# Kernel optimization log

Measured on AMD Instinct MI355X. Metric: run time of the kernel, lower is better.

Reference implementation:

```python
import jax, jax.numpy as jnp
import numpy as np

N, F_IN, HID, HEADS, NC, E, NG = 50000, 128, 64, 4, 8, 800000, 512


def setup_inputs() -> dict:
    key = jax.random.key(0)
    ks = jax.random.split(key, 16)
    x = jax.random.normal(ks[0], (N, F_IN), dtype=jnp.float32)
    # edges with src != dst so every node's incoming set is exactly {neighbors, self-loop}
    dst = jax.random.randint(ks[1], (E,), 0, N, dtype=jnp.int64)
    off = jax.random.randint(ks[2], (E,), 1, N, dtype=jnp.int64)
    src = (dst + off) % N
    edge_index = jnp.stack([src, dst])
    batch = jnp.sort(jax.random.randint(ks[3], (N,), 0, NG, dtype=jnp.int64))
    g = 1.0 / np.sqrt(F_IN)
    W1 = jax.random.uniform(ks[4], (F_IN, HEADS * HID), jnp.float32, -g, g)
    att_src1 = jax.random.normal(ks[5], (HEADS, HID), jnp.float32) * 0.1
    att_dst1 = jax.random.normal(ks[6], (HEADS, HID), jnp.float32) * 0.1
    b1 = jnp.zeros((HEADS * HID,), jnp.float32)
    g2 = 1.0 / np.sqrt(HEADS * HID)
    W2 = jax.random.uniform(ks[7], (HEADS * HID, HID), jnp.float32, -g2, g2)
    att_src2 = jax.random.normal(ks[8], (1, HID), jnp.float32) * 0.1
    att_dst2 = jax.random.normal(ks[9], (1, HID), jnp.float32) * 0.1
    b2 = jnp.zeros((HID,), jnp.float32)
    g3 = 1.0 / np.sqrt(HID)
    lin_w = jax.random.uniform(ks[10], (HID, NC), jnp.float32, -g3, g3)
    lin_b = jnp.zeros((NC,), jnp.float32)
    return dict(x=x, edge_index=edge_index, batch=batch, W1=W1, att_src1=att_src1,
                att_dst1=att_dst1, b1=b1, W2=W2, att_src2=att_src2, att_dst2=att_dst2,
                b2=b2, lin_w=lin_w, lin_b=lin_b)


def gat_layer(x, src, dst, W, att_s, att_d, bias, heads, out_ch):
    # PyG GATConv: h = x @ W, e_ij = LeakyReLU(a_s.h_j + a_d.h_i), softmax over dst groups
    h = (x @ W).reshape(-1, heads, out_ch)                    # [N,H,C]
    a_s = jnp.einsum('nhc,hc->nh', h, att_s)                  # [N,H]
    a_d = jnp.einsum('nhc,hc->nh', h, att_d)
    e = jax.nn.leaky_relu(a_s[src] + a_d[dst], 0.2)           # [Ef,H]
    m = jax.ops.segment_max(e, dst, num_segments=N)           # stable segment softmax
    ex = jnp.exp(e - m[dst])
    s = jax.ops.segment_sum(ex, dst, num_segments=N)
    alpha = ex / (s[dst] + 1e-16)                             # [Ef,H]
    msg = h[src] * alpha[:, :, None]                          # [Ef,H,C]
    out = jax.ops.segment_sum(msg, dst, num_segments=N)       # [N,H,C]
    return out.reshape(-1, heads * out_ch) + bias, alpha


def reference(x, edge_index, batch, W1, att_src1, att_dst1, b1,
              W2, att_src2, att_dst2, b2, lin_w, lin_b):
    loops = jnp.arange(N, dtype=edge_index.dtype)
    src = jnp.concatenate([edge_index[0], loops])             # add self-loops (PyG default)
    dst = jnp.concatenate([edge_index[1], loops])
    h, alpha1 = gat_layer(x, src, dst, W1, att_src1, att_dst1, b1, HEADS, HID)
    h = jax.nn.relu(h)
    # conv2 on edge_index_1 (already has self-loops; PyG remove+add is a no-op here)
    h, alpha2 = gat_layer(h, src, dst, W2, att_src2, att_dst2, b2, 1, HID)
    h = jax.nn.relu(h)
    sums = jax.ops.segment_sum(h, batch, num_segments=NG)     # global_mean_pool
    cnt = jax.ops.segment_sum(jnp.ones((N,), h.dtype), batch, num_segments=NG)
    pooled = sums / jnp.maximum(cnt, 1.0)[:, None]
    # dropout is identity in eval mode
    return pooled @ lin_w + lin_b
```

## Files before the change

### kernel.cpp

```cpp
#include <hip/hip_runtime.h>

#define F_IN 128
#define HID 64
#define HEADS 4
#define NC 8

typedef __bf16 bf16_t;
typedef bf16_t bf16x8 __attribute__((ext_vector_type(8)));
typedef float f32x4 __attribute__((ext_vector_type(4)));

union BF8 { bf16x8 v; ushort u[8]; };


__device__ __forceinline__ ushort f2bf(float f) {
    uint u = __float_as_uint(f);
    return (ushort)((u + 0x7fffu + ((u >> 16) & 1u)) >> 16);
}
__device__ __forceinline__ float bf2f(ushort h) {
    return __uint_as_float(((uint)h) << 16);
}
__device__ __forceinline__ float edgew(float e) {
    e = (e > 0.f) ? e : 0.2f * e;
    return __expf(e);
}


__global__ void k_init(int* __restrict__ deg, int N, int* __restrict__ counts, int NG) {
    int i = blockIdx.x * blockDim.x + threadIdx.x;
    if (i < N) deg[i] = 1;
    if (i < NG) counts[i] = 0;
}

__global__ void k_count(const int* __restrict__ ei, int E, int* __restrict__ deg,
                        const int* __restrict__ batch, int N, int* __restrict__ counts) {
    int i = blockIdx.x * blockDim.x + threadIdx.x;
    if (i < E) atomicAdd(&deg[ei[E + i]], 1);
    if (i < N) atomicAdd(&counts[batch[i]], 1);
}

__global__ __launch_bounds__(1024) void k_scan_part(const int* __restrict__ v,
                                                    int* __restrict__ excl,
                                                    int* __restrict__ bsum, int n) {
    __shared__ int buf[1024];
    int tid = threadIdx.x;
    int i = blockIdx.x * 1024 + tid;
    int val = (i < n) ? v[i] : 0;
    buf[tid] = val;
    __syncthreads();
    for (int off = 1; off < 1024; off <<= 1) {
        int t = (tid >= off) ? buf[tid - off] : 0;
        __syncthreads();
        buf[tid] += t;
        __syncthreads();
    }
    if (i < n) excl[i] = buf[tid] - val;
    if (tid == 1023) bsum[blockIdx.x] = buf[1023];
}

__global__ __launch_bounds__(1024) void k_scan_bsum(const int* __restrict__ bsum,
                                                    int* __restrict__ boff, int nb,
                                                    int* __restrict__ total_out) {
    __shared__ int buf[1024];
    int tid = threadIdx.x;
    int val = (tid < nb) ? bsum[tid] : 0;
    buf[tid] = val;
    __syncthreads();
    for (int off = 1; off < 1024; off <<= 1) {
        int t = (tid >= off) ? buf[tid - off] : 0;
        __syncthreads();
        buf[tid] += t;
        __syncthreads();
    }
    if (tid < nb) boff[tid] = buf[tid] - val;
    if (tid == 1023) total_out[0] = buf[1023];
}

__global__ void k_scan_add_self(int* __restrict__ rowstart, const int* __restrict__ boff,
                                int* __restrict__ cursor, int* __restrict__ csr, int n) {
    int i = blockIdx.x * blockDim.x + threadIdx.x;
    if (i < n) {
        int rs = rowstart[i] + boff[i >> 10];
        rowstart[i] = rs;
        csr[rs] = i;
        cursor[i] = 1;
    }
}

__global__ __launch_bounds__(1024) void k_scan(const int* __restrict__ v, int* __restrict__ excl, int n) {
    __shared__ int buf[1024];
    int tid = threadIdx.x;
    int val = (tid < n) ? v[tid] : 0;
    buf[tid] = val;
    __syncthreads();
    for (int off = 1; off < 1024; off <<= 1) {
        int t = (tid >= off) ? buf[tid - off] : 0;
        __syncthreads();
        buf[tid] += t;
        __syncthreads();
    }
    if (tid < n) excl[tid] = buf[tid] - val;
    if (tid == 1023) excl[n] = buf[1023];
}

__global__ void k_scatter(const int* __restrict__ ei, int E, const int* __restrict__ rowstart,
                          int* __restrict__ cursor, int* __restrict__ csr) {
    int e = blockIdx.x * blockDim.x + threadIdx.x;
    if (e < E) {
        int d = ei[E + e], s = ei[e];
        int pos = atomicAdd(&cursor[d], 1);
        csr[rowstart[d] + pos] = s;
    }
}

__global__ void k_pack(const float* __restrict__ W1, const float* __restrict__ W2,
                       ushort* __restrict__ w1hi, ushort* __restrict__ w1lo,
                       ushort* __restrict__ w2hi, ushort* __restrict__ w2lo) {
    int i = blockIdx.x * blockDim.x + threadIdx.x;
    if (i < 128 * 256) {
        int k = i >> 8, n = i & 255;
        int cy = n >> 7, ct = (n >> 4) & 7, c = n & 15, kc = k >> 5, ls = (k >> 3) & 3, j = k & 7;
        size_t off = ((((size_t)cy * 8 + ct) * 4 + kc) * 64 + (ls * 16 + c)) * 8 + j;
        float w = W1[i];
        ushort hi = f2bf(w);
        w1hi[off] = hi; w1lo[off] = f2bf(w - bf2f(hi));
    }
    if (i < 256 * 64) {
        int k = i >> 6, n = i & 63;
        int ct = n >> 4, c = n & 15, kc = k >> 5, ls = (k >> 3) & 3, j = k & 7;
        size_t off = (((size_t)ct * 8 + kc) * 64 + (ls * 16 + c)) * 8 + j;
        float w = W2[i];
        ushort hi = f2bf(w);
        w2hi[off] = hi; w2lo[off] = f2bf(w - bf2f(hi));
    }
}

__global__ __launch_bounds__(256) void k_gemm1(const float* __restrict__ x,
                                               const ushort* __restrict__ w1hi,
                                               const ushort* __restrict__ w1lo,
                                               const float* __restrict__ atts,
                                               const float* __restrict__ attd,
                                               ushort* __restrict__ h1b,
                                               float* __restrict__ as1, float* __restrict__ ad1,
                                               int N) {
    __shared__ __align__(16) ushort lhi[16384];
    __shared__ __align__(16) ushort llo[16384];
    int tid = threadIdx.x;
    int cy = blockIdx.y;
    {
        float4* dh = (float4*)lhi; const float4* sh = (const float4*)(w1hi + (size_t)cy * 16384);
        float4* dl = (float4*)llo; const float4* sl = (const float4*)(w1lo + (size_t)cy * 16384);
        #pragma unroll
        for (int i = 0; i < 8; i++) {
            dh[tid + i * 256] = sh[tid + i * 256];
            dl[tid + i * 256] = sl[tid + i * 256];
        }
    }
    __syncthreads();
    int w = tid >> 6, l = tid & 63;
    int lc = l & 15, lk = l >> 4;
    int rbase = blockIdx.x * 256 + w * 64;

    f32x4 acc[4][8];
    #pragma unroll
    for (int mt = 0; mt < 4; mt++)
        #pragma unroll
        for (int ct = 0; ct < 8; ct++) acc[mt][ct] = (f32x4){0.f, 0.f, 0.f, 0.f};

    #pragma unroll
    for (int kc = 0; kc < 4; kc++) {
        BF8 ahi[4], alo[4];
        #pragma unroll
        for (int mt = 0; mt < 4; mt++) {
            int row = rbase + mt * 16 + lc;
            float4 v0 = {0.f, 0.f, 0.f, 0.f}, v1 = v0;
            if (row < N) {
                const float* xp = x + (size_t)row * F_IN + kc * 32 + lk * 8;
                v0 = *(const float4*)xp; v1 = *(const float4*)(xp + 4);
            }
            float vals[8] = {v0.x, v0.y, v0.z, v0.w, v1.x, v1.y, v1.z, v1.w};
            #pragma unroll
            for (int j = 0; j < 8; j++) {
                ushort h = f2bf(vals[j]);
                ahi[mt].u[j] = h;
                alo[mt].u[j] = f2bf(vals[j] - bf2f(h));
            }
        }
        #pragma unroll
        for (int ct = 0; ct < 8; ct++) {
            int boff = ((ct * 4 + kc) * 64 + l) * 8;
            bf16x8 bhi = *(const bf16x8*)(lhi + boff);
            bf16x8 blo = *(const bf16x8*)(llo + boff);
            #pragma unroll
            for (int mt = 0; mt < 4; mt++) {
                acc[mt][ct] = __builtin_amdgcn_mfma_f32_16x16x32_bf16(ahi[mt].v, bhi, acc[mt][ct], 0, 0, 0);
                acc[mt][ct] = __builtin_amdgcn_mfma_f32_16x16x32_bf16(alo[mt].v, bhi, acc[mt][ct], 0, 0, 0);
                acc[mt][ct] = __builtin_amdgcn_mfma_f32_16x16x32_bf16(ahi[mt].v, blo, acc[mt][ct], 0, 0, 0);
            }
        }
    }
    #pragma unroll
    for (int mt = 0; mt < 4; mt++) {
        int rowb = rbase + mt * 16 + lk * 4;
        #pragma unroll
        for (int ct = 0; ct < 8; ct++) {
            int col = cy * 128 + ct * 16 + lc;
            #pragma unroll
            for (int r = 0; r < 4; r++) {
                int row = rowb + r;
                if (row < N) h1b[(size_t)row * 256 + col] = f2bf(acc[mt][ct][r]);
            }
        }
        #pragma unroll
        for (int hh = 0; hh < 2; hh++) {
            float s[4] = {0.f, 0.f, 0.f, 0.f}, d[4] = {0.f, 0.f, 0.f, 0.f};
            #pragma unroll
            for (int cq = 0; cq < 4; cq++) {
                int ct = hh * 4 + cq;
                int col = cy * 128 + ct * 16 + lc;
                float av = atts[col], dv = attd[col];
                #pragma unroll
                for (int r = 0; r < 4; r++) { s[r] += acc[mt][ct][r] * av; d[r] += acc[mt][ct][r] * dv; }
            }
            #pragma unroll
            for (int r = 0; r < 4; r++) {
                #pragma unroll
                for (int off = 1; off < 16; off <<= 1) {
                    s[r] += __shfl_xor(s[r], off);
                    d[r] += __shfl_xor(d[r], off);
                }
            }
            if (lc == 0) {
                int head = cy * 2 + hh;
                #pragma unroll
                for (int r = 0; r < 4; r++) {
                    int row = rowb + r;
                    if (row < N) { as1[row * 4 + head] = s[r]; ad1[row * 4 + head] = d[r]; }
                }
            }
        }
    }
}

__global__ __launch_bounds__(256) void k_gemm2(const float* __restrict__ xin,
                                               const ushort* __restrict__ w2hi,
                                               const ushort* __restrict__ w2lo,
                                               const float* __restrict__ atts,
                                               const float* __restrict__ attd,
                                               ushort* __restrict__ h2b,
                                               float* __restrict__ as2, float* __restrict__ ad2,
                                               int N) {
    __shared__ __align__(16) ushort lhi[16384];
    __shared__ __align__(16) ushort llo[16384];
    int tid = threadIdx.x;
    {
        float4* dh = (float4*)lhi; const float4* sh = (const float4*)w2hi;
        float4* dl = (float4*)llo; const float4* sl = (const float4*)w2lo;
        #pragma unroll
        for (int i = 0; i < 8; i++) {
            dh[tid + i * 256] = sh[tid + i * 256];
            dl[tid + i * 256] = sl[tid + i * 256];
        }
    }
    __syncthreads();
    int w = tid >> 6, l = tid & 63;
    int lc = l & 15, lk = l >> 4;
    int rbase = blockIdx.x * 256 + w * 64;

    f32x4 acc[4][4];
    #pragma unroll
    for (int mt = 0; mt < 4; mt++)
        #pragma unroll
        for (int ct = 0; ct < 4; ct++) acc[mt][ct] = (f32x4){0.f, 0.f, 0.f, 0.f};

    #pragma unroll
    for (int kc = 0; kc < 8; kc++) {
        BF8 ahi[4], alo[4];
        #pragma unroll
        for (int mt = 0; mt < 4; mt++) {
            int row = rbase + mt * 16 + lc;
            float4 v0 = {0.f, 0.f, 0.f, 0.f}, v1 = v0;
            if (row < N) {
                const float* xp = xin + (size_t)row * 256 + kc * 32 + lk * 8;
                v0 = *(const float4*)xp; v1 = *(const float4*)(xp + 4);
            }
            float vals[8] = {v0.x, v0.y, v0.z, v0.w, v1.x, v1.y, v1.z, v1.w};
            #pragma unroll
            for (int j = 0; j < 8; j++) {
                ushort h = f2bf(vals[j]);
                ahi[mt].u[j] = h;
                alo[mt].u[j] = f2bf(vals[j] - bf2f(h));
            }
        }
        #pragma unroll
        for (int ct = 0; ct < 4; ct++) {
            int boff = ((ct * 8 + kc) * 64 + l) * 8;
            bf16x8 bhi = *(const bf16x8*)(lhi + boff);
            bf16x8 blo = *(const bf16x8*)(llo + boff);
            #pragma unroll
            for (int mt = 0; mt < 4; mt++) {
                acc[mt][ct] = __builtin_amdgcn_mfma_f32_16x16x32_bf16(ahi[mt].v, bhi, acc[mt][ct], 0, 0, 0);
                acc[mt][ct] = __builtin_amdgcn_mfma_f32_16x16x32_bf16(alo[mt].v, bhi, acc[mt][ct], 0, 0, 0);
                acc[mt][ct] = __builtin_amdgcn_mfma_f32_16x16x32_bf16(ahi[mt].v, blo, acc[mt][ct], 0, 0, 0);
            }
        }
    }
    #pragma unroll
    for (int mt = 0; mt < 4; mt++) {
        int rowb = rbase + mt * 16 + lk * 4;
        #pragma unroll
        for (int ct = 0; ct < 4; ct++) {
            int col = ct * 16 + lc;
            #pragma unroll
            for (int r = 0; r < 4; r++) {
                int row = rowb + r;
                if (row < N) h2b[(size_t)row * 64 + col] = f2bf(acc[mt][ct][r]);
            }
        }
        float s[4] = {0.f, 0.f, 0.f, 0.f}, d[4] = {0.f, 0.f, 0.f, 0.f};
        #pragma unroll
        for (int ct = 0; ct < 4; ct++) {
            int col = ct * 16 + lc;
            float av = atts[col], dv = attd[col];
            #pragma unroll
            for (int r = 0; r < 4; r++) { s[r] += acc[mt][ct][r] * av; d[r] += acc[mt][ct][r] * dv; }
        }
        #pragma unroll
        for (int r = 0; r < 4; r++) {
            #pragma unroll
            for (int off = 1; off < 16; off <<= 1) {
                s[r] += __shfl_xor(s[r], off);
                d[r] += __shfl_xor(d[r], off);
            }
        }
        if (lc == 0) {
            #pragma unroll
            for (int r = 0; r < 4; r++) {
                int row = rowb + r;
                if (row < N) { as2[row] = s[r]; ad2[row] = d[r]; }
            }
        }
    }
}


__global__ __launch_bounds__(256) void k_agg1(const ushort* __restrict__ h1b,
                                              const float* __restrict__ as, const float* __restrict__ ad,
                                              const int* __restrict__ rowstart, const int* __restrict__ csr,
                                              const float* __restrict__ b1,
                                              float* __restrict__ out1, int N) {
    int n = blockIdx.x * 4 + (threadIdx.x >> 6);
    int lane = threadIdx.x & 63;
    if (n >= N) return;
    int head = lane >> 4;
    int coff = lane * 4;
    float adv = ad[n * 4 + head];
    int beg = rowstart[n], end = rowstart[n + 1];
    float a0 = 0.f, a1 = 0.f, a2 = 0.f, a3 = 0.f, ssum = 0.f;
    int j = beg;
    for (; j + 4 <= end; j += 4) {
        int s0 = csr[j + 0], s1 = csr[j + 1], s2 = csr[j + 2], s3 = csr[j + 3];
        float e0 = as[s0 * 4 + head], e1 = as[s1 * 4 + head];
        float e2 = as[s2 * 4 + head], e3 = as[s3 * 4 + head];
        ushort4 v0 = *(const ushort4*)(h1b + (size_t)s0 * 256 + coff);
        ushort4 v1 = *(const ushort4*)(h1b + (size_t)s1 * 256 + coff);
        ushort4 v2 = *(const ushort4*)(h1b + (size_t)s2 * 256 + coff);
        ushort4 v3 = *(const ushort4*)(h1b + (size_t)s3 * 256 + coff);
        float w0 = edgew(e0 + adv), w1 = edgew(e1 + adv);
        float w2 = edgew(e2 + adv), w3 = edgew(e3 + adv);
        ssum += (w0 + w1) + (w2 + w3);
        a0 += w0 * bf2f(v0.x) + w1 * bf2f(v1.x) + w2 * bf2f(v2.x) + w3 * bf2f(v3.x);
        a1 += w0 * bf2f(v0.y) + w1 * bf2f(v1.y) + w2 * bf2f(v2.y) + w3 * bf2f(v3.y);
        a2 += w0 * bf2f(v0.z) + w1 * bf2f(v1.z) + w2 * bf2f(v2.z) + w3 * bf2f(v3.z);
        a3 += w0 * bf2f(v0.w) + w1 * bf2f(v1.w) + w2 * bf2f(v2.w) + w3 * bf2f(v3.w);
    }
    for (; j < end; j++) {
        int s0 = csr[j];
        float w0 = edgew(as[s0 * 4 + head] + adv);
        ushort4 v0 = *(const ushort4*)(h1b + (size_t)s0 * 256 + coff);
        ssum += w0;
        a0 += w0 * bf2f(v0.x); a1 += w0 * bf2f(v0.y);
        a2 += w0 * bf2f(v0.z); a3 += w0 * bf2f(v0.w);
    }
    float inv = 1.f / ssum;
    float o0 = a0 * inv + b1[coff + 0];
    float o1 = a1 * inv + b1[coff + 1];
    float o2 = a2 * inv + b1[coff + 2];
    float o3 = a3 * inv + b1[coff + 3];
    float4 o;
    o.x = o0 > 0.f ? o0 : 0.f; o.y = o1 > 0.f ? o1 : 0.f;
    o.z = o2 > 0.f ? o2 : 0.f; o.w = o3 > 0.f ? o3 : 0.f;
    *(float4*)(out1 + (size_t)n * 256 + coff) = o;
}

__global__ __launch_bounds__(256) void k_agg2(const ushort* __restrict__ h2b,
                                              const float* __restrict__ as, const float* __restrict__ ad,
                                              const int* __restrict__ rowstart, const int* __restrict__ csr,
                                              const float* __restrict__ b2,
                                              float* __restrict__ out2, int N) {
    int n = blockIdx.x * 4 + (threadIdx.x >> 6);
    int lane = threadIdx.x & 63;
    if (n >= N) return;
    float adv = ad[n];
    int beg = rowstart[n], end = rowstart[n + 1];
    float acc = 0.f, ssum = 0.f;
    int j = beg;
    for (; j + 4 <= end; j += 4) {
        int s0 = csr[j + 0], s1 = csr[j + 1], s2 = csr[j + 2], s3 = csr[j + 3];
        float e0 = as[s0], e1 = as[s1], e2 = as[s2], e3 = as[s3];
        ushort v0 = h2b[(size_t)s0 * 64 + lane];
        ushort v1 = h2b[(size_t)s1 * 64 + lane];
        ushort v2 = h2b[(size_t)s2 * 64 + lane];
        ushort v3 = h2b[(size_t)s3 * 64 + lane];
        float w0 = edgew(e0 + adv), w1 = edgew(e1 + adv);
        float w2 = edgew(e2 + adv), w3 = edgew(e3 + adv);
        ssum += (w0 + w1) + (w2 + w3);
        acc += w0 * bf2f(v0) + w1 * bf2f(v1) + w2 * bf2f(v2) + w3 * bf2f(v3);
    }
    for (; j < end; j++) {
        int s0 = csr[j];
        float w0 = edgew(as[s0] + adv);
        ssum += w0;
        acc += w0 * bf2f(h2b[(size_t)s0 * 64 + lane]);
    }
    float o = acc / ssum + b2[lane];
    out2[(size_t)n * 64 + lane] = o > 0.f ? o : 0.f;
}


__global__ __launch_bounds__(64) void k_pool(const float* __restrict__ out2,
                                             const int* __restrict__ gstart,
                                             const float* __restrict__ lin_w,
                                             const float* __restrict__ lin_b,
                                             float* __restrict__ out, int NG) {
    __shared__ float mean[64];
    int g = blockIdx.x;
    int lane = threadIdx.x;
    int beg = gstart[g], end = gstart[g + 1];
    float s = 0.f;
    for (int n = beg; n < end; n++) s += out2[(size_t)n * 64 + lane];
    float cnt = (float)(end - beg);
    mean[lane] = s / fmaxf(cnt, 1.f);
    __syncthreads();
    if (lane < NC) {
        float acc = lin_b[lane];
        #pragma unroll
        for (int c = 0; c < 64; c++) acc += mean[c] * lin_w[c * NC + lane];
        out[g * NC + lane] = acc;
    }
}


extern "C" void kernel_launch(void* const* d_in, const int* in_sizes, int n_in,
                              void* d_out, int out_size, void* d_ws, size_t ws_size,
                              hipStream_t stream) {
    const float* x      = (const float*)d_in[0];
    const int*   ei     = (const int*)d_in[1];
    const int*   batch  = (const int*)d_in[2];
    const float* W1     = (const float*)d_in[3];
    const float* att_s1 = (const float*)d_in[4];
    const float* att_d1 = (const float*)d_in[5];
    const float* b1     = (const float*)d_in[6];
    const float* W2     = (const float*)d_in[7];
    const float* att_s2 = (const float*)d_in[8];
    const float* att_d2 = (const float*)d_in[9];
    const float* b2     = (const float*)d_in[10];
    const float* lin_w  = (const float*)d_in[11];
    const float* lin_b  = (const float*)d_in[12];
    float* out = (float*)d_out;

    const int N  = in_sizes[0] / F_IN;
    const int E  = in_sizes[1] / 2;
    const int NG = out_size / NC;
    const int NE = E + N;
    const int NB = (N + 1023) / 1024;

    char* p = (char*)d_ws;
    auto alloc = [&](size_t bytes) { char* r = p; p += (bytes + 255) & ~(size_t)255; return r; };
    ushort* h1b     = (ushort*)alloc(sizeof(ushort) * (size_t)N * 256);
    float*  out1    = (float*)alloc(sizeof(float) * (size_t)N * 256);
    ushort* h2b     = (ushort*)alloc(sizeof(ushort) * (size_t)N * 64);
    float*  out2    = (float*)alloc(sizeof(float) * (size_t)N * 64);
    float*  as1     = (float*)alloc(sizeof(float) * (size_t)N * 4);
    float*  ad1     = (float*)alloc(sizeof(float) * (size_t)N * 4);
    float*  as2     = (float*)alloc(sizeof(float) * (size_t)N);
    float*  ad2     = (float*)alloc(sizeof(float) * (size_t)N);
    int*    rowstart= (int*)alloc(sizeof(int) * (size_t)(N + 1));
    int*    itmp    = (int*)alloc(sizeof(int) * (size_t)N);
    int*    csr     = (int*)alloc(sizeof(int) * (size_t)NE);
    int*    counts  = (int*)alloc(sizeof(int) * (size_t)NG);
    int*    gstart  = (int*)alloc(sizeof(int) * (size_t)(NG + 1));
    int*    bsum    = (int*)alloc(sizeof(int) * 1024);
    int*    boff    = (int*)alloc(sizeof(int) * 1024);
    ushort* w1hi    = (ushort*)alloc(sizeof(ushort) * 32768);
    ushort* w1lo    = (ushort*)alloc(sizeof(ushort) * 32768);
    ushort* w2hi    = (ushort*)alloc(sizeof(ushort) * 16384);
    ushort* w2lo    = (ushort*)alloc(sizeof(ushort) * 16384);

    int bs = 256;
    k_pack<<<128, 256, 0, stream>>>(W1, W2, w1hi, w1lo, w2hi, w2lo);
    k_init<<<(N + bs - 1) / bs, bs, 0, stream>>>(itmp, N, counts, NG);
    k_count<<<(E + bs - 1) / bs, bs, 0, stream>>>(ei, E, itmp, batch, N, counts);
    k_scan_part<<<NB, 1024, 0, stream>>>(itmp, rowstart, bsum, N);
    k_scan_bsum<<<1, 1024, 0, stream>>>(bsum, boff, NB, rowstart + N);
    k_scan_add_self<<<(N + 1023) / 1024, 1024, 0, stream>>>(rowstart, boff, itmp, csr, N);
    k_scan<<<1, 1024, 0, stream>>>(counts, gstart, NG);
    k_scatter<<<(E + bs - 1) / bs, bs, 0, stream>>>(ei, E, rowstart, itmp, csr);

    k_gemm1<<<dim3((N + 255) / 256, 2), 256, 0, stream>>>(x, w1hi, w1lo, att_s1, att_d1, h1b, as1, ad1, N);
    k_agg1<<<(N + 3) / 4, 256, 0, stream>>>(h1b, as1, ad1, rowstart, csr, b1, out1, N);

    k_gemm2<<<(N + 255) / 256, 256, 0, stream>>>(out1, w2hi, w2lo, att_s2, att_d2, h2b, as2, ad2, N);
    k_agg2<<<(N + 3) / 4, 256, 0, stream>>>(h2b, as2, ad2, rowstart, csr, b2, out2, N);

    k_pool<<<NG, 64, 0, stream>>>(out2, gstart, lin_w, lin_b, out, NG);
}
```

Measured before the change: 323.8 us.

## Store layer-1 output as bf16, fuse setup kernels, deepen gather unroll

Layer-1 aggregation now writes its ReLU output as bf16 instead of fp32. This halves that intermediate's write and read traffic and lets gemm2 load bf16 directly, dropping the on-the-fly hi/lo split and one of three MFMAs per tile. The weight pack and init kernels are merged, and the two small scans run as two blocks of one launch, which removes two launches. The aggregation gather loops are unrolled to 8 edges to keep more loads in flight. The cost is lower precision on the layer-2 input, since it is no longer split-bf16 compensated.

```diff
diff --git a/kernel.cpp b/kernel.cpp
--- a/kernel.cpp
+++ b/kernel.cpp
@@ -24,11 +24,29 @@
     return __expf(e);
 }
 
-
-__global__ void k_init(int* __restrict__ deg, int N, int* __restrict__ counts, int NG) {
+__global__ void k_setup(const float* __restrict__ W1, const float* __restrict__ W2,
+                        ushort* __restrict__ w1hi, ushort* __restrict__ w1lo,
+                        ushort* __restrict__ w2hi, ushort* __restrict__ w2lo,
+                        int* __restrict__ deg, int N, int* __restrict__ counts, int NG) {
     int i = blockIdx.x * blockDim.x + threadIdx.x;
     if (i < N) deg[i] = 1;
     if (i < NG) counts[i] = 0;
+    if (i < 128 * 256) {
+        int k = i >> 8, n = i & 255;
+        int cy = n >> 7, ct = (n >> 4) & 7, c = n & 15, kc = k >> 5, ls = (k >> 3) & 3, j = k & 7;
+        size_t off = ((((size_t)cy * 8 + ct) * 4 + kc) * 64 + (ls * 16 + c)) * 8 + j;
+        float w = W1[i];
+        ushort hi = f2bf(w);
+        w1hi[off] = hi; w1lo[off] = f2bf(w - bf2f(hi));
+    }
+    if (i < 256 * 64) {
+        int k = i >> 6, n = i & 63;
+        int ct = n >> 4, c = n & 15, kc = k >> 5, ls = (k >> 3) & 3, j = k & 7;
+        size_t off = (((size_t)ct * 8 + kc) * 64 + (ls * 16 + c)) * 8 + j;
+        float w = W2[i];
+        ushort hi = f2bf(w);
+        w2hi[off] = hi; w2lo[off] = f2bf(w - bf2f(hi));
+    }
 }
 
 __global__ void k_count(const int* __restrict__ ei, int E, int* __restrict__ deg,
@@ -57,12 +75,16 @@
     if (tid == 1023) bsum[blockIdx.x] = buf[1023];
 }
 
-__global__ __launch_bounds__(1024) void k_scan_bsum(const int* __restrict__ bsum,
-                                                    int* __restrict__ boff, int nb,
-                                                    int* __restrict__ total_out) {
+__global__ __launch_bounds__(1024) void k_scan_small2(const int* __restrict__ bsum,
+                                                      int* __restrict__ boff, int nb,
+                                                      int* __restrict__ total_out,
+                                                      const int* __restrict__ counts,
+                                                      int* __restrict__ gstart, int ng) {
     __shared__ int buf[1024];
     int tid = threadIdx.x;
-    int val = (tid < nb) ? bsum[tid] : 0;
+    const int* src = (blockIdx.x == 0) ? bsum : counts;
+    int cnt = (blockIdx.x == 0) ? nb : ng;
+    int val = (tid < cnt) ? src[tid] : 0;
     buf[tid] = val;
     __syncthreads();
     for (int off = 1; off < 1024; off <<= 1) {
@@ -71,8 +93,13 @@
         buf[tid] += t;
         __syncthreads();
     }
-    if (tid < nb) boff[tid] = buf[tid] - val;
-    if (tid == 1023) total_out[0] = buf[1023];
+    if (blockIdx.x == 0) {
+        if (tid < cnt) boff[tid] = buf[tid] - val;
+        if (tid == 1023) total_out[0] = buf[1023];
+    } else {
+        if (tid < cnt) gstart[tid] = buf[tid] - val;
+        if (tid == 1023) gstart[ng] = buf[1023];
+    }
 }
 
 __global__ void k_scan_add_self(int* __restrict__ rowstart, const int* __restrict__ boff,
@@ -86,22 +113,6 @@
     }
 }
 
-__global__ __launch_bounds__(1024) void k_scan(const int* __restrict__ v, int* __restrict__ excl, int n) {
-    __shared__ int buf[1024];
-    int tid = threadIdx.x;
-    int val = (tid < n) ? v[tid] : 0;
-    buf[tid] = val;
-    __syncthreads();
-    for (int off = 1; off < 1024; off <<= 1) {
-        int t = (tid >= off) ? buf[tid - off] : 0;
-        __syncthreads();
-        buf[tid] += t;
-        __syncthreads();
-    }
-    if (tid < n) excl[tid] = buf[tid] - val;
-    if (tid == 1023) excl[n] = buf[1023];
-}
-
 __global__ void k_scatter(const int* __restrict__ ei, int E, const int* __restrict__ rowstart,
                           int* __restrict__ cursor, int* __restrict__ csr) {
     int e = blockIdx.x * blockDim.x + threadIdx.x;
@@ -109,28 +120,6 @@
         int d = ei[E + e], s = ei[e];
         int pos = atomicAdd(&cursor[d], 1);
         csr[rowstart[d] + pos] = s;
-    }
-}
-
-__global__ void k_pack(const float* __restrict__ W1, const float* __restrict__ W2,
-                       ushort* __restrict__ w1hi, ushort* __restrict__ w1lo,
-                       ushort* __restrict__ w2hi, ushort* __restrict__ w2lo) {
-    int i = blockIdx.x * blockDim.x + threadIdx.x;
-    if (i < 128 * 256) {
-        int k = i >> 8, n = i & 255;
-        int cy = n >> 7, ct = (n >> 4) & 7, c = n & 15, kc = k >> 5, ls = (k >> 3) & 3, j = k & 7;
-        size_t off = ((((size_t)cy * 8 + ct) * 4 + kc) * 64 + (ls * 16 + c)) * 8 + j;
-        float w = W1[i];
-        ushort hi = f2bf(w);
-        w1hi[off] = hi; w1lo[off] = f2bf(w - bf2f(hi));
-    }
-    if (i < 256 * 64) {
-        int k = i >> 6, n = i & 63;
-        int ct = n >> 4, c = n & 15, kc = k >> 5, ls = (k >> 3) & 3, j = k & 7;
-        size_t off = (((size_t)ct * 8 + kc) * 64 + (ls * 16 + c)) * 8 + j;
-        float w = W2[i];
-        ushort hi = f2bf(w);
-        w2hi[off] = hi; w2lo[off] = f2bf(w - bf2f(hi));
     }
 }
 
@@ -241,7 +230,7 @@
     }
 }
 
-__global__ __launch_bounds__(256) void k_gemm2(const float* __restrict__ xin,
+__global__ __launch_bounds__(256) void k_gemm2(const ushort* __restrict__ xin,
                                                const ushort* __restrict__ w2hi,
                                                const ushort* __restrict__ w2lo,
                                                const float* __restrict__ atts,
@@ -274,21 +263,15 @@
 
     #pragma unroll
     for (int kc = 0; kc < 8; kc++) {
-        BF8 ahi[4], alo[4];
+        BF8 a[4];
         #pragma unroll
         for (int mt = 0; mt < 4; mt++) {
             int row = rbase + mt * 16 + lc;
-            float4 v0 = {0.f, 0.f, 0.f, 0.f}, v1 = v0;
             if (row < N) {
-                const float* xp = xin + (size_t)row * 256 + kc * 32 + lk * 8;
-                v0 = *(const float4*)xp; v1 = *(const float4*)(xp + 4);
-            }
-            float vals[8] = {v0.x, v0.y, v0.z, v0.w, v1.x, v1.y, v1.z, v1.w};
-            #pragma unroll
-            for (int j = 0; j < 8; j++) {
-                ushort h = f2bf(vals[j]);
-                ahi[mt].u[j] = h;
-                alo[mt].u[j] = f2bf(vals[j] - bf2f(h));
+                a[mt].v = *(const bf16x8*)(xin + (size_t)row * 256 + kc * 32 + lk * 8);
+            } else {
+                #pragma unroll
+                for (int j = 0; j < 8; j++) a[mt].u[j] = 0;
             }
         }
         #pragma unroll
@@ -298,9 +281,8 @@
             bf16x8 blo = *(const bf16x8*)(llo + boff);
             #pragma unroll
             for (int mt = 0; mt < 4; mt++) {
-                acc[mt][ct] = __builtin_amdgcn_mfma_f32_16x16x32_bf16(ahi[mt].v, bhi, acc[mt][ct], 0, 0, 0);
-                acc[mt][ct] = __builtin_amdgcn_mfma_f32_16x16x32_bf16(alo[mt].v, bhi, acc[mt][ct], 0, 0, 0);
-                acc[mt][ct] = __builtin_amdgcn_mfma_f32_16x16x32_bf16(ahi[mt].v, blo, acc[mt][ct], 0, 0, 0);
+                acc[mt][ct] = __builtin_amdgcn_mfma_f32_16x16x32_bf16(a[mt].v, bhi, acc[mt][ct], 0, 0, 0);
+                acc[mt][ct] = __builtin_amdgcn_mfma_f32_16x16x32_bf16(a[mt].v, blo, acc[mt][ct], 0, 0, 0);
             }
         }
     }
@@ -347,7 +329,7 @@
                                               const float* __restrict__ as, const float* __restrict__ ad,
                                               const int* __restrict__ rowstart, const int* __restrict__ csr,
                                               const float* __restrict__ b1,
-                                              float* __restrict__ out1, int N) {
+                                              ushort* __restrict__ out1b, int N) {
     int n = blockIdx.x * 4 + (threadIdx.x >> 6);
     int lane = threadIdx.x & 63;
     if (n >= N) return;
@@ -357,39 +339,40 @@
     int beg = rowstart[n], end = rowstart[n + 1];
     float a0 = 0.f, a1 = 0.f, a2 = 0.f, a3 = 0.f, ssum = 0.f;
     int j = beg;
-    for (; j + 4 <= end; j += 4) {
-        int s0 = csr[j + 0], s1 = csr[j + 1], s2 = csr[j + 2], s3 = csr[j + 3];
-        float e0 = as[s0 * 4 + head], e1 = as[s1 * 4 + head];
-        float e2 = as[s2 * 4 + head], e3 = as[s3 * 4 + head];
-        ushort4 v0 = *(const ushort4*)(h1b + (size_t)s0 * 256 + coff);
-        ushort4 v1 = *(const ushort4*)(h1b + (size_t)s1 * 256 + coff);
-        ushort4 v2 = *(const ushort4*)(h1b + (size_t)s2 * 256 + coff);
-        ushort4 v3 = *(const ushort4*)(h1b + (size_t)s3 * 256 + coff);
-        float w0 = edgew(e0 + adv), w1 = edgew(e1 + adv);
-        float w2 = edgew(e2 + adv), w3 = edgew(e3 + adv);
-        ssum += (w0 + w1) + (w2 + w3);
-        a0 += w0 * bf2f(v0.x) + w1 * bf2f(v1.x) + w2 * bf2f(v2.x) + w3 * bf2f(v3.x);
-        a1 += w0 * bf2f(v0.y) + w1 * bf2f(v1.y) + w2 * bf2f(v2.y) + w3 * bf2f(v3.y);
-        a2 += w0 * bf2f(v0.z) + w1 * bf2f(v1.z) + w2 * bf2f(v2.z) + w3 * bf2f(v3.z);
-        a3 += w0 * bf2f(v0.w) + w1 * bf2f(v1.w) + w2 * bf2f(v2.w) + w3 * bf2f(v3.w);
+    for (; j + 8 <= end; j += 8) {
+        int s[8];
+        #pragma unroll
+        for (int i = 0; i < 8; i++) s[i] = csr[j + i];
+        float e[8];
+        #pragma unroll
+        for (int i = 0; i < 8; i++) e[i] = as[s[i] * 4 + head];
+        ushort4 hv[8];
+        #pragma unroll
+        for (int i = 0; i < 8; i++) hv[i] = *(const ushort4*)(h1b + (size_t)s[i] * 256 + coff);
+        #pragma unroll
+        for (int i = 0; i < 8; i++) {
+            float wv = edgew(e[i] + adv);
+            ssum += wv;
+            a0 += wv * bf2f(hv[i].x); a1 += wv * bf2f(hv[i].y);
+            a2 += wv * bf2f(hv[i].z); a3 += wv * bf2f(hv[i].w);
+        }
     }
     for (; j < end; j++) {
         int s0 = csr[j];
-        float w0 = edgew(as[s0 * 4 + head] + adv);
+        float wv = edgew(as[s0 * 4 + head] + adv);
         ushort4 v0 = *(const ushort4*)(h1b + (size_t)s0 * 256 + coff);
-        ssum += w0;
-        a0 += w0 * bf2f(v0.x); a1 += w0 * bf2f(v0.y);
-        a2 += w0 * bf2f(v0.z); a3 += w0 * bf2f(v0.w);
+        ssum += wv;
+        a0 += wv * bf2f(v0.x); a1 += wv * bf2f(v0.y);
+        a2 += wv * bf2f(v0.z); a3 += wv * bf2f(v0.w);
     }
     float inv = 1.f / ssum;
-    float o0 = a0 * inv + b1[coff + 0];
-    float o1 = a1 * inv + b1[coff + 1];
-    float o2 = a2 * inv + b1[coff + 2];
-    float o3 = a3 * inv + b1[coff + 3];
-    float4 o;
-    o.x = o0 > 0.f ? o0 : 0.f; o.y = o1 > 0.f ? o1 : 0.f;
-    o.z = o2 > 0.f ? o2 : 0.f; o.w = o3 > 0.f ? o3 : 0.f;
-    *(float4*)(out1 + (size_t)n * 256 + coff) = o;
+    float o0 = fmaxf(a0 * inv + b1[coff + 0], 0.f);
+    float o1 = fmaxf(a1 * inv + b1[coff + 1], 0.f);
+    float o2 = fmaxf(a2 * inv + b1[coff + 2], 0.f);
+    float o3 = fmaxf(a3 * inv + b1[coff + 3], 0.f);
+    ushort4 o;
+    o.x = f2bf(o0); o.y = f2bf(o1); o.z = f2bf(o2); o.w = f2bf(o3);
+    *(ushort4*)(out1b + (size_t)n * 256 + coff) = o;
 }
 
 __global__ __launch_bounds__(256) void k_agg2(const ushort* __restrict__ h2b,
@@ -404,23 +387,28 @@
     int beg = rowstart[n], end = rowstart[n + 1];
     float acc = 0.f, ssum = 0.f;
     int j = beg;
-    for (; j + 4 <= end; j += 4) {
-        int s0 = csr[j + 0], s1 = csr[j + 1], s2 = csr[j + 2], s3 = csr[j + 3];
-        float e0 = as[s0], e1 = as[s1], e2 = as[s2], e3 = as[s3];
-        ushort v0 = h2b[(size_t)s0 * 64 + lane];
-        ushort v1 = h2b[(size_t)s1 * 64 + lane];
-        ushort v2 = h2b[(size_t)s2 * 64 + lane];
-        ushort v3 = h2b[(size_t)s3 * 64 + lane];
-        float w0 = edgew(e0 + adv), w1 = edgew(e1 + adv);
-        float w2 = edgew(e2 + adv), w3 = edgew(e3 + adv);
-        ssum += (w0 + w1) + (w2 + w3);
-        acc += w0 * bf2f(v0) + w1 * bf2f(v1) + w2 * bf2f(v2) + w3 * bf2f(v3);
+    for (; j + 8 <= end; j += 8) {
+        int s[8];
+        #pragma unroll
+        for (int i = 0; i < 8; i++) s[i] = csr[j + i];
+        float e[8];
+        #pragma unroll
+        for (int i = 0; i < 8; i++) e[i] = as[s[i]];
+        ushort hv[8];
+        #pragma unroll
+        for (int i = 0; i < 8; i++) hv[i] = h2b[(size_t)s[i] * 64 + lane];
+        #pragma unroll
+        for (int i = 0; i < 8; i++) {
+            float wv = edgew(e[i] + adv);
+            ssum += wv;
+            acc += wv * bf2f(hv[i]);
+        }
     }
     for (; j < end; j++) {
         int s0 = csr[j];
-        float w0 = edgew(as[s0] + adv);
-        ssum += w0;
-        acc += w0 * bf2f(h2b[(size_t)s0 * 64 + lane]);
+        float wv = edgew(as[s0] + adv);
+        ssum += wv;
+        acc += wv * bf2f(h2b[(size_t)s0 * 64 + lane]);
     }
     float o = acc / ssum + b2[lane];
     out2[(size_t)n * 64 + lane] = o > 0.f ? o : 0.f;
@@ -477,7 +465,7 @@
     char* p = (char*)d_ws;
     auto alloc = [&](size_t bytes) { char* r = p; p += (bytes + 255) & ~(size_t)255; return r; };
     ushort* h1b     = (ushort*)alloc(sizeof(ushort) * (size_t)N * 256);
-    float*  out1    = (float*)alloc(sizeof(float) * (size_t)N * 256);
+    ushort* out1b   = (ushort*)alloc(sizeof(ushort) * (size_t)N * 256);
     ushort* h2b     = (ushort*)alloc(sizeof(ushort) * (size_t)N * 64);
     float*  out2    = (float*)alloc(sizeof(float) * (size_t)N * 64);
     float*  as1     = (float*)alloc(sizeof(float) * (size_t)N * 4);
@@ -497,19 +485,18 @@
     ushort* w2lo    = (ushort*)alloc(sizeof(ushort) * 16384);
 
     int bs = 256;
-    k_pack<<<128, 256, 0, stream>>>(W1, W2, w1hi, w1lo, w2hi, w2lo);
-    k_init<<<(N + bs - 1) / bs, bs, 0, stream>>>(itmp, N, counts, NG);
+    k_setup<<<(N + bs - 1) / bs, bs, 0, stream>>>(W1, W2, w1hi, w1lo, w2hi, w2lo,
+                                                  itmp, N, counts, NG);
     k_count<<<(E + bs - 1) / bs, bs, 0, stream>>>(ei, E, itmp, batch, N, counts);
     k_scan_part<<<NB, 1024, 0, stream>>>(itmp, rowstart, bsum, N);
-    k_scan_bsum<<<1, 1024, 0, stream>>>(bsum, boff, NB, rowstart + N);
+    k_scan_small2<<<2, 1024, 0, stream>>>(bsum, boff, NB, rowstart + N, counts, gstart, NG);
     k_scan_add_self<<<(N + 1023) / 1024, 1024, 0, stream>>>(rowstart, boff, itmp, csr, N);
-    k_scan<<<1, 1024, 0, stream>>>(counts, gstart, NG);
     k_scatter<<<(E + bs - 1) / bs, bs, 0, stream>>>(ei, E, rowstart, itmp, csr);
 
     k_gemm1<<<dim3((N + 255) / 256, 2), 256, 0, stream>>>(x, w1hi, w1lo, att_s1, att_d1, h1b, as1, ad1, N);
-    k_agg1<<<(N + 3) / 4, 256, 0, stream>>>(h1b, as1, ad1, rowstart, csr, b1, out1, N);
-
-    k_gemm2<<<(N + 255) / 256, 256, 0, stream>>>(out1, w2hi, w2lo, att_s2, att_d2, h2b, as2, ad2, N);
+    k_agg1<<<(N + 3) / 4, 256, 0, stream>>>(h1b, as1, ad1, rowstart, csr, b1, out1b, N);
+
+    k_gemm2<<<(N + 255) / 256, 256, 0, stream>>>(out1b, w2hi, w2lo, att_s2, att_d2, h2b, as2, ad2, N);
     k_agg2<<<(N + 3) / 4, 256, 0, stream>>>(h2b, as2, ad2, rowstart, csr, b2, out2, N);
 
     k_pool<<<NG, 64, 0, stream>>>(out2, gstart, lin_w, lin_b, out, NG);
```

Result: no change. 321.4 us (-0.7%).
